# Kernel tuning notes

Hardware: AMD Instinct MI355X
Metric: run time of the kernel (lower is better)

## Reference

```python
import jax, jax.numpy as jnp
import numpy as np

BS, NE, NN, CIN, H, D = 8, 4800, 4981, 3, 128, 6
EPG = 19200
NEDGE = BS * EPG
N = BS * NE

PARAM_NAMES = [
    'enc_cw1','enc_cb1','enc_cw2','enc_cb2','enc_cw3','enc_clng','enc_clnb',
    'enc_ew1','enc_eb1','enc_ew2','enc_eb2','enc_ew3','enc_elng','enc_elnb',
    'p_ew1','p_eb1','p_ew2','p_eb2','p_ew3','p_elng','p_elnb',
    'p_nw1','p_nb1','p_nw2','p_nb2','p_nw3','p_nlng','p_nlnb',
    'dec_uw1','dec_ub1','dec_uw2','dec_ub2','dec_uw3','dec_ulng','dec_ulnb',
    'dec_cw1','dec_cb1','dec_cw2','dec_cb2','dec_cw3']


def setup_inputs():
    key = jax.random.key(0)
    ks = iter(jax.random.split(key, 64))
    def nrm(shape, s=0.1):
        return jax.random.normal(next(ks), shape, jnp.float32) * s
    inp = {}
    inp['x'] = jax.random.normal(next(ks), (BS * NN, CIN), jnp.float32)
    inp['elem_conn'] = jax.random.randint(next(ks), (NE, 4), 0, NN)
    inp['edge_index'] = jax.random.randint(next(ks), (2, NEDGE), 0, N)
    inp['enc_cw1'] = nrm((CIN, 4, 1)); inp['enc_cb1'] = nrm((CIN, 1), 0.01)
    inp['enc_cw2'] = nrm((CIN, 1, 1)); inp['enc_cb2'] = nrm((CIN, 1), 0.01)
    inp['enc_cw3'] = nrm((CIN, 1, 1))
    inp['enc_clng'] = jnp.ones((CIN, 1)); inp['enc_clnb'] = jnp.zeros((CIN, 1))
    inp['enc_ew1'] = nrm((CIN, H)); inp['enc_eb1'] = nrm((H,), 0.01)
    inp['enc_ew2'] = nrm((H, H)); inp['enc_eb2'] = nrm((H,), 0.01)
    inp['enc_ew3'] = nrm((H, H))
    inp['enc_elng'] = jnp.ones((H,)); inp['enc_elnb'] = jnp.zeros((H,))
    inp['p_ew1'] = nrm((D, 2 * H, H)); inp['p_eb1'] = nrm((D, H), 0.01)
    inp['p_ew2'] = nrm((D, H, H)); inp['p_eb2'] = nrm((D, H), 0.01)
    inp['p_ew3'] = nrm((D, H, H))
    inp['p_elng'] = jnp.ones((D, H)); inp['p_elnb'] = jnp.zeros((D, H))
    inp['p_nw1'] = nrm((D, 2 * H, H)); inp['p_nb1'] = nrm((D, H), 0.01)
    inp['p_nw2'] = nrm((D, H, H)); inp['p_nb2'] = nrm((D, H), 0.01)
    inp['p_nw3'] = nrm((D, H, H))
    inp['p_nlng'] = jnp.ones((D, H)); inp['p_nlnb'] = jnp.zeros((D, H))
    inp['dec_uw1'] = nrm((H, 1, 4)); inp['dec_ub1'] = nrm((H, 4), 0.01)
    inp['dec_uw2'] = nrm((H, 4, 4)); inp['dec_ub2'] = nrm((H, 4), 0.01)
    inp['dec_uw3'] = nrm((H, 4, 4))
    inp['dec_ulng'] = jnp.ones((H, 4)); inp['dec_ulnb'] = jnp.zeros((H, 4))
    inp['dec_cw1'] = nrm((H, CIN)); inp['dec_cb1'] = nrm((CIN,), 0.01)
    inp['dec_cw2'] = nrm((CIN, CIN)); inp['dec_cb2'] = nrm((CIN,), 0.01)
    inp['dec_cw3'] = nrm((CIN, CIN))
    return inp


def lrelu(x):
    return jnp.where(x >= 0, x, 0.2 * x)


def ln(x, g, b, axis=-1):
    m = jnp.mean(x, axis=axis, keepdims=True)
    v = jnp.var(x, axis=axis, keepdims=True)
    return (x - m) / jnp.sqrt(v + 1e-5) * g + b


def mlp(x, w1, b1, w2, b2, w3):
    h = lrelu(x @ w1 + b1)
    h = lrelu(h @ w2 + b2)
    return h @ w3


def _forward(fl, elem_conn, edge_index):
    x = fl[0]
    P = dict(zip(PARAM_NAMES, fl[1:]))
    # ---- Encoder: MeshCNN gather (4 mesh nodes per element) + per-channel MLP 4->1 ----
    xg = x.reshape(BS, NN, CIN)[:, elem_conn]                  # (BS, NE, 4, CIN)
    h = lrelu(jnp.einsum('beic,cio->beoc', xg, P['enc_cw1']) + P['enc_cb1'].T[None, None])
    h = lrelu(jnp.einsum('beic,cio->beoc', h, P['enc_cw2']) + P['enc_cb2'].T[None, None])
    h = jnp.einsum('beic,cio->beoc', h, P['enc_cw3'])
    h = ln(h, P['enc_clng'].T[None, None], P['enc_clnb'].T[None, None], axis=2)  # LayerNorm(1)
    h = h[:, :, 0, :].reshape(N, CIN)
    h = ln(mlp(h, P['enc_ew1'], P['enc_eb1'], P['enc_ew2'], P['enc_eb2'], P['enc_ew3']),
           P['enc_elng'], P['enc_elnb'])                       # (N, H)
    # ---- Processor: D GraphNet blocks, edge MLP + scatter-add + node MLP ----
    src, dest = edge_index[0], edge_index[1]
    stacked = (P['p_ew1'], P['p_eb1'], P['p_ew2'], P['p_eb2'], P['p_ew3'], P['p_elng'], P['p_elnb'],
               P['p_nw1'], P['p_nb1'], P['p_nw2'], P['p_nb2'], P['p_nw3'], P['p_nlng'], P['p_nlnb'])
    def step(hc, p):
        ew1, eb1, ew2, eb2, ew3, eg, ebv, nw1, nb1, nw2, nb2, nw3, ng, nbv = p
        msg = jnp.concatenate([hc[dest], hc[src]], axis=-1)    # (NEDGE, 2H)
        m = ln(mlp(msg, ew1, eb1, ew2, eb2, ew3), eg, ebv)
        aggr = jax.ops.segment_sum(m, dest, num_segments=N)
        hn = ln(mlp(jnp.concatenate([hc, aggr], axis=-1), nw1, nb1, nw2, nb2, nw3), ng, nbv)
        return hn, None
    h, _ = jax.lax.scan(step, h, stacked)
    # ---- Decoder: per-channel upsample 1->4 then index_add back to mesh nodes ----
    u = h.reshape(BS, NE, H)[:, :, None, :]                    # (BS, NE, 1, H)
    u = lrelu(jnp.einsum('beic,cio->beoc', u, P['dec_uw1']) + P['dec_ub1'].T[None, None])
    u = lrelu(jnp.einsum('beic,cio->beoc', u, P['dec_uw2']) + P['dec_ub2'].T[None, None])
    u = jnp.einsum('beic,cio->beoc', u, P['dec_uw3'])
    u = ln(u, P['dec_ulng'].T[None, None], P['dec_ulnb'].T[None, None], axis=2)  # (BS, NE, 4, H)
    out = jnp.zeros((BS, NN, H), u.dtype).at[:, elem_conn.reshape(-1)].add(u.reshape(BS, NE * 4, H))
    out = out.reshape(BS * NN, H)
    o = lrelu(out @ P['dec_cw1'] + P['dec_cb1'])
    o = lrelu(o @ P['dec_cw2'] + P['dec_cb2'])
    return o @ P['dec_cw3']


def reference(x, elem_conn, edge_index,
              enc_cw1, enc_cb1, enc_cw2, enc_cb2, enc_cw3, enc_clng, enc_clnb,
              enc_ew1, enc_eb1, enc_ew2, enc_eb2, enc_ew3, enc_elng, enc_elnb,
              p_ew1, p_eb1, p_ew2, p_eb2, p_ew3, p_elng, p_elnb,
              p_nw1, p_nb1, p_nw2, p_nb2, p_nw3, p_nlng, p_nlnb,
              dec_uw1, dec_ub1, dec_uw2, dec_ub2, dec_uw3, dec_ulng, dec_ulnb,
              dec_cw1, dec_cb1, dec_cw2, dec_cb2, dec_cw3):
    fl = (x, enc_cw1, enc_cb1, enc_cw2, enc_cb2, enc_cw3, enc_clng, enc_clnb,
          enc_ew1, enc_eb1, enc_ew2, enc_eb2, enc_ew3, enc_elng, enc_elnb,
          p_ew1, p_eb1, p_ew2, p_eb2, p_ew3, p_elng, p_elnb,
          p_nw1, p_nb1, p_nw2, p_nb2, p_nw3, p_nlng, p_nlnb,
          dec_uw1, dec_ub1, dec_uw2, dec_ub2, dec_uw3, dec_ulng, dec_ulnb,
          dec_cw1, dec_cb1, dec_cw2, dec_cb2, dec_cw3)
    return _forward(fl, elem_conn, edge_index)
```

## Files before the change

### kernel.cpp

```cpp
#include <hip/hip_runtime.h>
#include <hip/hip_fp16.h>
#include <math.h>

#define BS    8
#define NE    4800
#define NN    4981
#define CIN   3
#define HD    128
#define DBLK  6
#define NEDGE 153600
#define NTOT  38400
#define NMESH (BS*NN)
#define NNP   5120
#define EM    128
#define TROWS 256

#define UW1T  0
#define UB1T  512
#define UW2T  1024
#define UB2T  3072
#define UW3T  3584
#define ULNGT 5632
#define ULNBT 6144
#define DWT_N 6656

typedef _Float16 f16;
typedef _Float16 f16x8 __attribute__((ext_vector_type(8)));
typedef float f32x4 __attribute__((ext_vector_type(4)));

__device__ __forceinline__ float lrelu(float x) { return x >= 0.0f ? x : 0.2f * x; }

__global__ __launch_bounds__(128)
void enc_msg0_kernel(const float* __restrict__ clnb,
                     const float* __restrict__ ew1, const float* __restrict__ eb1,
                     const float* __restrict__ ew2, const float* __restrict__ eb2,
                     const float* __restrict__ ew3,
                     const float* __restrict__ g, const float* __restrict__ b,
                     float* __restrict__ hv0,
                     const float* __restrict__ pew1, const float* __restrict__ peb1,
                     const float* __restrict__ pew2, const float* __restrict__ peb2,
                     const float* __restrict__ pew3,
                     const float* __restrict__ pg, const float* __restrict__ pb,
                     float* __restrict__ m0) {
    __shared__ float s1[HD], s2[HD], s3[HD], hv[HD];
    int j = threadIdx.x;
    float a = eb1[j];
    for (int c = 0; c < CIN; ++c) a += clnb[c] * ew1[c * HD + j];
    s1[j] = lrelu(a);
    __syncthreads();
    a = eb2[j];
    for (int k = 0; k < HD; ++k) a += s1[k] * ew2[k * HD + j];
    s2[j] = lrelu(a);
    __syncthreads();
    a = 0.0f;
    for (int k = 0; k < HD; ++k) a += s2[k] * ew3[k * HD + j];
    s3[j] = a;
    __syncthreads();
    float m = 0.0f;
    for (int k = 0; k < HD; ++k) m += s3[k];
    m *= (1.0f / HD);
    float v = 0.0f;
    for (int k = 0; k < HD; ++k) { float d = s3[k] - m; v += d * d; }
    v *= (1.0f / HD);
    float rs = 1.0f / sqrtf(v + 1e-5f);
    float h0 = (s3[j] - m) * rs * g[j] + b[j];
    hv0[j] = h0;
    hv[j] = h0;
    __syncthreads();
    a = peb1[j];
    for (int k = 0; k < HD; ++k) a += hv[k] * (pew1[k * HD + j] + pew1[(k + HD) * HD + j]);
    s1[j] = lrelu(a);
    __syncthreads();
    a = peb2[j];
    for (int k = 0; k < HD; ++k) a += s1[k] * pew2[k * HD + j];
    s2[j] = lrelu(a);
    __syncthreads();
    a = 0.0f;
    for (int k = 0; k < HD; ++k) a += s2[k] * pew3[k * HD + j];
    s3[j] = a;
    __syncthreads();
    m = 0.0f;
    for (int k = 0; k < HD; ++k) m += s3[k];
    m *= (1.0f / HD);
    v = 0.0f;
    for (int k = 0; k < HD; ++k) { float d = s3[k] - m; v += d * d; }
    v *= (1.0f / HD);
    rs = 1.0f / sqrtf(v + 1e-5f);
    m0[j] = (s3[j] - m) * rs * pg[j] + pb[j];
}

__global__ __launch_bounds__(256)
void conv_all_kernel(const float* __restrict__ ew1, const float* __restrict__ ew2,
                     const float* __restrict__ ew3,
                     const float* __restrict__ nw1, const float* __restrict__ nw2,
                     const float* __restrict__ nw3, f16* __restrict__ wbuf,
                     const float* __restrict__ eb1, f16* __restrict__ eb16,
                     const float* __restrict__ uw1, const float* __restrict__ ub1,
                     const float* __restrict__ uw2, const float* __restrict__ ub2,
                     const float* __restrict__ uw3, const float* __restrict__ ulng,
                     const float* __restrict__ ulnb, float* __restrict__ dwt,
                     int* __restrict__ degIota,
                     int* __restrict__ zdeg, int* __restrict__ zcur,
                     int* __restrict__ zmdeg, int* __restrict__ zmcur) {
    int b = blockIdx.x;
    int tid = threadIdx.x;
    if (b == 48) {
        for (int i = tid; i < DBLK * HD; i += 256)
            eb16[i] = (f16)eb1[i];
        degIota[tid] = tid;
        return;
    }
    if (b == 49) {
        for (int idx = tid; idx < 512; idx += 256) {
            int o = idx >> 7, c = idx & 127;
            dwt[UW1T + idx] = uw1[c * 4 + o];
            dwt[UB1T + idx] = ub1[c * 4 + o];
            dwt[UB2T + idx] = ub2[c * 4 + o];
            dwt[ULNGT + idx] = ulng[c * 4 + o];
            dwt[ULNBT + idx] = ulnb[c * 4 + o];
        }
        for (int idx = tid; idx < 2048; idx += 256) {
            int io = idx >> 7, c = idx & 127;
            dwt[UW2T + idx] = uw2[c * 16 + io];
            dwt[UW3T + idx] = uw3[c * 16 + io];
        }
        return;
    }
    if (b >= 50) {
        uint4 z = {0, 0, 0, 0};
        for (int idx = (b - 50) * 256 + tid; idx < 21760; idx += 8 * 256) {
            if (idx < 9600)       ((uint4*)zdeg)[idx] = z;
            else if (idx < 19200) ((uint4*)zcur)[idx - 9600] = z;
            else if (idx < 20480) ((uint4*)zmdeg)[idx - 19200] = z;
            else                  ((uint4*)zmcur)[idx - 20480] = z;
        }
        return;
    }
    int d = b >> 3, m = b & 7;
    const float* src;
    switch (m) {
        case 0: src = ew1 + (size_t)d * 2 * HD * HD; break;
        case 1: src = ew1 + (size_t)d * 2 * HD * HD + HD * HD; break;
        case 2: src = ew2 + (size_t)d * HD * HD; break;
        case 3: src = ew3 + (size_t)d * HD * HD; break;
        case 4: src = nw1 + (size_t)d * 2 * HD * HD; break;
        case 5: src = nw1 + (size_t)d * 2 * HD * HD + HD * HD; break;
        case 6: src = nw2 + (size_t)d * HD * HD; break;
        default: src = nw3 + (size_t)d * HD * HD; break;
    }
    f16* out = wbuf + (size_t)b * HD * HD;
    for (int idx = tid; idx < HD * HD; idx += 256) {
        int n = idx >> 7, k = idx & 127;
        out[idx] = (f16)src[k * HD + n];
    }
}

#define EHB (NEDGE / 256)
#define MHB (NE * 4 / 256)
#define ESB (NTOT / 256)
#define MSB (NNP / 256)

__global__ __launch_bounds__(256)
void prep_hist(const int* __restrict__ e_dst, const int* __restrict__ conn,
               int* __restrict__ deg, int* __restrict__ mdeg) {
    int b = blockIdx.x;
    if (b < EHB) {
        int e = b * 256 + threadIdx.x;
        atomicAdd(&deg[e_dst[e]], 1);
    } else {
        int idx = (b - EHB) * 256 + threadIdx.x;
        atomicAdd(&mdeg[conn[idx]], 1);
    }
}

__device__ __forceinline__ void scan1_body(const int* __restrict__ deg,
                                           int* __restrict__ rowptr,
                                           int* __restrict__ bsum, int bi) {
    __shared__ int s[256];
    int i = bi * 256 + threadIdx.x;
    int v = deg[i];
    s[threadIdx.x] = v;
    __syncthreads();
    for (int off = 1; off < 256; off <<= 1) {
        int t = (threadIdx.x >= off) ? s[threadIdx.x - off] : 0;
        __syncthreads();
        s[threadIdx.x] += t;
        __syncthreads();
    }
    rowptr[i] = s[threadIdx.x] - v;
    if (threadIdx.x == 255) bsum[bi] = s[255];
}

__global__ __launch_bounds__(256)
void prep_scan1(const int* __restrict__ deg, int* __restrict__ rowptr,
                int* __restrict__ bsum,
                const int* __restrict__ mdeg, int* __restrict__ mrow,
                int* __restrict__ mbsum) {
    int b = blockIdx.x;
    if (b < ESB) scan1_body(deg, rowptr, bsum, b);
    else         scan1_body(mdeg, mrow, mbsum, b - ESB);
}

__global__ __launch_bounds__(256)
void prep_scan3(int* __restrict__ rowptr, const int* __restrict__ bsum,
                int* __restrict__ mrow, const int* __restrict__ mbsum) {
    __shared__ int sb[256];
    int b = blockIdx.x;
    int tid = threadIdx.x;
    if (b < ESB) {
        sb[tid] = (tid < b) ? bsum[tid] : 0;
        __syncthreads();
        for (int off = 128; off >= 1; off >>= 1) {
            if (tid < off) sb[tid] += sb[tid + off];
            __syncthreads();
        }
        rowptr[b * 256 + tid] += sb[0];
    } else {
        int bb = b - ESB;
        sb[tid] = (tid < bb) ? mbsum[tid] : 0;
        __syncthreads();
        for (int off = 128; off >= 1; off >>= 1) {
            if (tid < off) sb[tid] += sb[tid + off];
            __syncthreads();
        }
        mrow[bb * 256 + tid] += sb[0];
    }
}

__global__ __launch_bounds__(256)
void prep_scatter(const int* __restrict__ dest, const int* __restrict__ srcv,
                  const int* __restrict__ rowptr, int* __restrict__ cursor,
                  int* __restrict__ dsorted, int* __restrict__ ssorted,
                  const int* __restrict__ conn, const int* __restrict__ mrow,
                  int* __restrict__ mcur, int* __restrict__ mslot,
                  const int* __restrict__ deg,
                  int* __restrict__ ddegs, int* __restrict__ sdegs) {
    int b = blockIdx.x;
    if (b < EHB) {
        int e = b * 256 + threadIdx.x;
        int d = dest[e];
        int s = srcv[e];
        int pos = rowptr[d] + atomicAdd(&cursor[d], 1);
        dsorted[pos] = d;
        ssorted[pos] = s;
        ddegs[pos] = deg[d];
        sdegs[pos] = deg[s];
    } else {
        int idx = (b - EHB) * 256 + threadIdx.x;
        int nd = conn[idx];
        int pos = mrow[nd] + atomicAdd(&mcur[nd], 1);
        mslot[pos] = idx;
    }
}

template <int NT>
__device__ __forceinline__ void stage_w(const f16* __restrict__ Wg, f16 (*Bt)[HD + 8],
                                        int tid) {
    #pragma unroll
    for (int t = 0; t < 2048 / NT; ++t) {
        int idx = tid + t * NT;
        int r = idx >> 4, c = (idx & 15) * 8;
        *(uint4*)(&Bt[r][c]) = *(const uint4*)(Wg + (size_t)r * HD + c);
    }
}

__device__ __forceinline__ void mfma_pass(const f16 (*A)[HD + 8], const f16 (*Bt)[HD + 8],
                                          int rt_base, int ct_base, int ln, int quad,
                                          f32x4 acc[2][4]) {
    #pragma unroll
    for (int ks = 0; ks < 4; ++ks) {
        int kb = ks * 32 + quad * 8;
        f16x8 a0 = *(const f16x8*)(&A[rt_base + ln][kb]);
        f16x8 a1 = *(const f16x8*)(&A[rt_base + 16 + ln][kb]);
        #pragma unroll
        for (int c = 0; c < 4; ++c) {
            f16x8 b = *(const f16x8*)(&Bt[ct_base + c * 16 + ln][kb]);
            acc[0][c] = __builtin_amdgcn_mfma_f32_16x16x32_f16(a0, b, acc[0][c], 0, 0, 0);
            acc[1][c] = __builtin_amdgcn_mfma_f32_16x16x32_f16(a1, b, acc[1][c], 0, 0, 0);
        }
    }
}

__global__ __launch_bounds__(512, 4)
void gn_edge(const f16* __restrict__ P1, const f16* __restrict__ P2,
             const int* __restrict__ dsorted, const int* __restrict__ ssorted,
             const f16* __restrict__ W2, const f16* __restrict__ W3,
             const f16* __restrict__ b1h, const float* __restrict__ b2,
             const float* __restrict__ g, const float* __restrict__ bln,
             f16* __restrict__ msg) {
    __shared__ __align__(16) f16 As[EM][HD + 8];
    __shared__ __align__(16) f16 Bt[HD][HD + 8];
    __shared__ float red[EM][2][2];

    const int tid = threadIdx.x;
    const int base = blockIdx.x * EM;
    const int wave = tid >> 6, lane = tid & 63;
    const int ln = lane & 15, quad = lane >> 4;
    const int rt_base = (wave >> 1) * 32;
    const int ct_base = (wave & 1) * 64;
    const int half = wave & 1;
    const int r0 = tid >> 4;
    const int cg = (tid & 15) * 8;

    const f16 k02s = (f16)0.2f;
    const f16x8 k02 = {k02s, k02s, k02s, k02s, k02s, k02s, k02s, k02s};

    int dI[4], sI[4];
    #pragma unroll
    for (int it = 0; it < 4; ++it) {
        dI[it] = dsorted[base + r0 + it * 32];
        sI[it] = ssorted[base + r0 + it * 32];
    }
    stage_w<512>(W2, Bt, tid);
    const f16x8 bb = *(const f16x8*)(b1h + cg);
    #pragma unroll
    for (int it = 0; it < 4; ++it) {
        f16x8 p1 = *(const f16x8*)(P1 + (size_t)dI[it] * HD + cg);
        f16x8 p2 = *(const f16x8*)(P2 + (size_t)sI[it] * HD + cg);
        f16x8 s = p1 + p2 + bb;
        *(f16x8*)(&As[r0 + it * 32][cg]) = __builtin_elementwise_max(s, s * k02);
    }
    __syncthreads();

    f32x4 acc[2][4];

    #pragma unroll
    for (int c = 0; c < 4; ++c) {
        float bj = b2[ct_base + c * 16 + ln];
        f32x4 bv = {bj, bj, bj, bj};
        acc[0][c] = bv; acc[1][c] = bv;
    }
    mfma_pass(As, Bt, rt_base, ct_base, ln, quad, acc);
    __syncthreads();
    stage_w<512>(W3, Bt, tid);
    #pragma unroll
    for (int i = 0; i < 2; ++i)
        #pragma unroll
        for (int c = 0; c < 4; ++c)
            #pragma unroll
            for (int r = 0; r < 4; ++r)
                As[rt_base + i * 16 + quad * 4 + r][ct_base + c * 16 + ln] =
                    (f16)lrelu(acc[i][c][r]);
    __syncthreads();

    #pragma unroll
    for (int c = 0; c < 4; ++c) { f32x4 z = {0,0,0,0}; acc[0][c] = z; acc[1][c] = z; }
    mfma_pass(As, Bt, rt_base, ct_base, ln, quad, acc);

    #pragma unroll
    for (int i = 0; i < 2; ++i)
        #pragma unroll
        for (int r = 0; r < 4; ++r) {
            float s = acc[i][0][r] + acc[i][1][r] + acc[i][2][r] + acc[i][3][r];
            float q = acc[i][0][r] * acc[i][0][r] + acc[i][1][r] * acc[i][1][r] +
                      acc[i][2][r] * acc[i][2][r] + acc[i][3][r] * acc[i][3][r];
            s += __shfl_xor(s, 1); q += __shfl_xor(q, 1);
            s += __shfl_xor(s, 2); q += __shfl_xor(q, 2);
            s += __shfl_xor(s, 4); q += __shfl_xor(q, 4);
            s += __shfl_xor(s, 8); q += __shfl_xor(q, 8);
            if (ln == 0) {
                int row = rt_base + i * 16 + quad * 4 + r;
                red[row][half][0] = s;
                red[row][half][1] = q;
            }
        }
    __syncthreads();

    float gv[4], bv[4];
    #pragma unroll
    for (int c = 0; c < 4; ++c) {
        int col = ct_base + c * 16 + ln;
        gv[c] = g[col]; bv[c] = bln[col];
    }
    #pragma unroll
    for (int i = 0; i < 2; ++i)
        #pragma unroll
        for (int r = 0; r < 4; ++r) {
            int row = rt_base + i * 16 + quad * 4 + r;
            float s = red[row][0][0] + red[row][1][0];
            float q = red[row][0][1] + red[row][1][1];
            float m = s * (1.0f / HD);
            float var = q * (1.0f / HD) - m * m;
            float rs = 1.0f / sqrtf(var + 1e-5f);
            #pragma unroll
            for (int c = 0; c < 4; ++c) {
                int col = ct_base + c * 16 + ln;
                float v = (acc[i][c][r] - m) * rs * gv[c] + bv[c];
                msg[(size_t)(base + row) * HD + col] = (f16)v;
            }
        }
}

template <int AGGR, bool PROD, bool DECF, bool HTAB>
__global__ __launch_bounds__(256, 3)
void gn_node(f16* __restrict__ h16, const f16* __restrict__ msg,
             const int* __restrict__ rowptr, const int* __restrict__ deg,
             const float* __restrict__ m0, const float* __restrict__ hv0,
             const f16* __restrict__ htab,
             const f16* __restrict__ W1a, const f16* __restrict__ W1b,
             const f16* __restrict__ W2, const f16* __restrict__ W3,
             const float* __restrict__ b1, const float* __restrict__ b2,
             const float* __restrict__ g, const float* __restrict__ bln,
             const f16* __restrict__ nW1a, const f16* __restrict__ nW1b,
             f16* __restrict__ P1, f16* __restrict__ P2,
             const float* __restrict__ dwt, f16* __restrict__ uval) {
    __shared__ __align__(16) f16 As[64][HD + 8];
    __shared__ __align__(16) f16 Bt[HD][HD + 8];
    __shared__ float red[64][2][2];

    const int tid = threadIdx.x;
    const int base = blockIdx.x * 64;
    const int wave = tid >> 6, lane = tid & 63;
    const int ln = lane & 15, quad = lane >> 4;
    const int rt_base = (wave >> 1) * 32;
    const int ct_base = (wave & 1) * 64;
    const int half = wave & 1;

    f16x8 hreg[4];
    #pragma unroll
    for (int t = 0; t < 4; ++t) {
        int r = (tid >> 4) + t * 16;
        int c = (tid & 15) * 8;
        if (AGGR == 0) {
            f16x8 hz;
            #pragma unroll
            for (int u = 0; u < 8; ++u) hz[u] = (f16)hv0[c + u];
            hreg[t] = hz;
            float sc = (float)deg[base + r];
            f16x8 o;
            #pragma unroll
            for (int u = 0; u < 8; ++u) o[u] = (f16)(sc * m0[c + u]);
            *(f16x8*)(&As[r][c]) = o;
        } else {
            if (HTAB)
                hreg[t] = *(const f16x8*)(htab + (size_t)deg[base + r] * HD + c);
            else
                hreg[t] = *(const f16x8*)(h16 + (size_t)(base + r) * HD + c);
            int rp = rowptr[base + r], dg = deg[base + r];
            float a[8] = {0, 0, 0, 0, 0, 0, 0, 0};
            int j = 0;
            for (; j + 4 <= dg; j += 4) {
                f16x8 v0 = *(const f16x8*)(msg + (size_t)(rp + j) * HD + c);
                f16x8 v1 = *(const f16x8*)(msg + (size_t)(rp + j + 1) * HD + c);
                f16x8 v2 = *(const f16x8*)(msg + (size_t)(rp + j + 2) * HD + c);
                f16x8 v3 = *(const f16x8*)(msg + (size_t)(rp + j + 3) * HD + c);
                #pragma unroll
                for (int u = 0; u < 8; ++u)
                    a[u] += ((float)v0[u] + (float)v1[u]) + ((float)v2[u] + (float)v3[u]);
            }
            for (; j < dg; ++j) {
                f16x8 mv = *(const f16x8*)(msg + (size_t)(rp + j) * HD + c);
                #pragma unroll
                for (int u = 0; u < 8; ++u) a[u] += (float)mv[u];
            }
            f16x8 o;
            #pragma unroll
            for (int u = 0; u < 8; ++u) o[u] = (f16)a[u];
            *(f16x8*)(&As[r][c]) = o;
        }
    }
    stage_w<256>(W1b, Bt, tid);
    __syncthreads();

    f32x4 acc[2][4];
    #pragma unroll
    for (int c = 0; c < 4; ++c) {
        float bj = b1[ct_base + c * 16 + ln];
        f32x4 bb = {bj, bj, bj, bj};
        acc[0][c] = bb; acc[1][c] = bb;
    }
    mfma_pass(As, Bt, rt_base, ct_base, ln, quad, acc);
    __syncthreads();

    #pragma unroll
    for (int t = 0; t < 4; ++t) {
        int r = (tid >> 4) + t * 16;
        int c = (tid & 15) * 8;
        *(f16x8*)(&As[r][c]) = hreg[t];
    }
    stage_w<256>(W1a, Bt, tid);
    __syncthreads();
    mfma_pass(As, Bt, rt_base, ct_base, ln, quad, acc);
    __syncthreads();

    stage_w<256>(W2, Bt, tid);
    #pragma unroll
    for (int i = 0; i < 2; ++i)
        #pragma unroll
        for (int c = 0; c < 4; ++c)
            #pragma unroll
            for (int r = 0; r < 4; ++r)
                As[rt_base + i * 16 + quad * 4 + r][ct_base + c * 16 + ln] =
                    (f16)lrelu(acc[i][c][r]);
    __syncthreads();

    #pragma unroll
    for (int c = 0; c < 4; ++c) {
        float bj = b2[ct_base + c * 16 + ln];
        f32x4 bb = {bj, bj, bj, bj};
        acc[0][c] = bb; acc[1][c] = bb;
    }
    mfma_pass(As, Bt, rt_base, ct_base, ln, quad, acc);
    __syncthreads();
    stage_w<256>(W3, Bt, tid);
    #pragma unroll
    for (int i = 0; i < 2; ++i)
        #pragma unroll
        for (int c = 0; c < 4; ++c)
            #pragma unroll
            for (int r = 0; r < 4; ++r)
                As[rt_base + i * 16 + quad * 4 + r][ct_base + c * 16 + ln] =
                    (f16)lrelu(acc[i][c][r]);
    __syncthreads();

    #pragma unroll
    for (int c = 0; c < 4; ++c) { f32x4 z = {0,0,0,0}; acc[0][c] = z; acc[1][c] = z; }
    mfma_pass(As, Bt, rt_base, ct_base, ln, quad, acc);

    #pragma unroll
    for (int i = 0; i < 2; ++i)
        #pragma unroll
        for (int r = 0; r < 4; ++r) {
            float s = acc[i][0][r] + acc[i][1][r] + acc[i][2][r] + acc[i][3][r];
            float q = acc[i][0][r] * acc[i][0][r] + acc[i][1][r] * acc[i][1][r] +
                      acc[i][2][r] * acc[i][2][r] + acc[i][3][r] * acc[i][3][r];
            s += __shfl_xor(s, 1); q += __shfl_xor(q, 1);
            s += __shfl_xor(s, 2); q += __shfl_xor(q, 2);
            s += __shfl_xor(s, 4); q += __shfl_xor(q, 4);
            s += __shfl_xor(s, 8); q += __shfl_xor(q, 8);
            if (ln == 0) {
                int row = rt_base + i * 16 + quad * 4 + r;
                red[row][half][0] = s;
                red[row][half][1] = q;
            }
        }
    __syncthreads();

    float gv[4], bv[4];
    #pragma unroll
    for (int c = 0; c < 4; ++c) {
        int col = ct_base + c * 16 + ln;
        gv[c] = g[col]; bv[c] = bln[col];
    }

    if (!DECF) {
        #pragma unroll
        for (int i = 0; i < 2; ++i)
            #pragma unroll
            for (int r = 0; r < 4; ++r) {
                int row = rt_base + i * 16 + quad * 4 + r;
                float s = red[row][0][0] + red[row][1][0];
                float q = red[row][0][1] + red[row][1][1];
                float m = s * (1.0f / HD);
                float var = q * (1.0f / HD) - m * m;
                float rs = 1.0f / sqrtf(var + 1e-5f);
                #pragma unroll
                for (int c = 0; c < 4; ++c) {
                    int col = ct_base + c * 16 + ln;
                    float v = (acc[i][c][r] - m) * rs * gv[c] + bv[c];
                    f16 hv = (f16)v;
                    h16[(size_t)(base + row) * HD + col] = hv;
                    if (PROD) As[row][col] = hv;
                }
            }
    } else {
        float mm[2][4], rr[2][4];
        #pragma unroll
        for (int i = 0; i < 2; ++i)
            #pragma unroll
            for (int r = 0; r < 4; ++r) {
                int row = rt_base + i * 16 + quad * 4 + r;
                float s = red[row][0][0] + red[row][1][0];
                float q = red[row][0][1] + red[row][1][1];
                float m = s * (1.0f / HD);
                float var = q * (1.0f / HD) - m * m;
                mm[i][r] = m;
                rr[i][r] = 1.0f / sqrtf(var + 1e-5f);
            }
        #pragma unroll
        for (int c = 0; c < 4; ++c) {
            int col = ct_base + c * 16 + ln;
            float w1v[4], wb1[4], wb2[4], lg4[4], lb4[4];
            #pragma unroll
            for (int o = 0; o < 4; ++o) {
                w1v[o] = dwt[UW1T + o * 128 + col];
                wb1[o] = dwt[UB1T + o * 128 + col];
                wb2[o] = dwt[UB2T + o * 128 + col];
                lg4[o] = dwt[ULNGT + o * 128 + col];
                lb4[o] = dwt[ULNBT + o * 128 + col];
            }
            float w2v[16], w3v[16];
            #pragma unroll
            for (int io = 0; io < 16; ++io) {
                w2v[io] = dwt[UW2T + io * 128 + col];
                w3v[io] = dwt[UW3T + io * 128 + col];
            }
            #pragma unroll
            for (int i = 0; i < 2; ++i)
                #pragma unroll
                for (int r = 0; r < 4; ++r) {
                    int row = rt_base + i * 16 + quad * 4 + r;
                    float v = (acc[i][c][r] - mm[i][r]) * rr[i][r] * gv[c] + bv[c];
                    float s = (float)(f16)v;
                    float u1[4], u2[4], u3[4];
                    #pragma unroll
                    for (int o = 0; o < 4; ++o)
                        u1[o] = lrelu(s * w1v[o] + wb1[o]);
                    #pragma unroll
                    for (int o = 0; o < 4; ++o) {
                        float a = wb2[o];
                        #pragma unroll
                        for (int i2 = 0; i2 < 4; ++i2) a += u1[i2] * w2v[i2 * 4 + o];
                        u2[o] = lrelu(a);
                    }
                    #pragma unroll
                    for (int o = 0; o < 4; ++o) {
                        float a = 0.f;
                        #pragma unroll
                        for (int i2 = 0; i2 < 4; ++i2) a += u2[i2] * w3v[i2 * 4 + o];
                        u3[o] = a;
                    }
                    float m4 = 0.25f * (u3[0] + u3[1] + u3[2] + u3[3]);
                    float var4 = 0.f;
                    #pragma unroll
                    for (int o = 0; o < 4; ++o) { float d = u3[o] - m4; var4 += d * d; }
                    var4 *= 0.25f;
                    float rs4 = 1.0f / sqrtf(var4 + 1e-5f);
                    size_t ub = (size_t)(base + row) * 4 * HD + col;
                    #pragma unroll
                    for (int o = 0; o < 4; ++o)
                        uval[ub + (size_t)o * HD] =
                            (f16)((u3[o] - m4) * rs4 * lg4[o] + lb4[o]);
                }
        }
    }

    if (PROD) {
        __syncthreads();
        stage_w<256>(nW1a, Bt, tid);
        __syncthreads();
        #pragma unroll
        for (int c = 0; c < 4; ++c) { f32x4 z = {0,0,0,0}; acc[0][c] = z; acc[1][c] = z; }
        mfma_pass(As, Bt, rt_base, ct_base, ln, quad, acc);
        #pragma unroll
        for (int i = 0; i < 2; ++i)
            #pragma unroll
            for (int c = 0; c < 4; ++c)
                #pragma unroll
                for (int r = 0; r < 4; ++r)
                    P1[(size_t)(base + rt_base + i * 16 + quad * 4 + r) * HD +
                       ct_base + c * 16 + ln] = (f16)acc[i][c][r];
        __syncthreads();
        stage_w<256>(nW1b, Bt, tid);
        __syncthreads();
        #pragma unroll
        for (int c = 0; c < 4; ++c) { f32x4 z = {0,0,0,0}; acc[0][c] = z; acc[1][c] = z; }
        mfma_pass(As, Bt, rt_base, ct_base, ln, quad, acc);
        #pragma unroll
        for (int i = 0; i < 2; ++i)
            #pragma unroll
            for (int c = 0; c < 4; ++c)
                #pragma unroll
                for (int r = 0; r < 4; ++r)
                    P2[(size_t)(base + rt_base + i * 16 + quad * 4 + r) * HD +
                       ct_base + c * 16 + ln] = (f16)acc[i][c][r];
    }
}

__global__ __launch_bounds__(256)
void dec_gather_out(const f16* __restrict__ uval,
                    const int* __restrict__ mrow, const int* __restrict__ mdeg,
                    const int* __restrict__ mslot,
                    const float* __restrict__ cw1, const float* __restrict__ cb1,
                    const float* __restrict__ cw2, const float* __restrict__ cb2,
                    const float* __restrict__ cw3,
                    float* __restrict__ o, int nrows) {
    int r = blockIdx.x * 4 + (threadIdx.x >> 6);
    if (r >= nrows) return;
    int lane = threadIdx.x & 63;
    int b = r / NN, n = r - b * NN;
    int rp = mrow[n], dg = mdeg[n];
    size_t boff = (size_t)b * NE * 4;
    float a0 = 0.f, a1 = 0.f;
    int j = 0;
    for (; j + 4 <= dg; j += 4) {
        int s0 = mslot[rp + j], s1 = mslot[rp + j + 1];
        int s2 = mslot[rp + j + 2], s3 = mslot[rp + j + 3];
        const f16* u0 = uval + (boff + s0) * HD + lane * 2;
        const f16* u1 = uval + (boff + s1) * HD + lane * 2;
        const f16* u2 = uval + (boff + s2) * HD + lane * 2;
        const f16* u3 = uval + (boff + s3) * HD + lane * 2;
        float b00 = (float)u0[0], b01 = (float)u0[1];
        float b10 = (float)u1[0], b11 = (float)u1[1];
        float b20 = (float)u2[0], b21 = (float)u2[1];
        float b30 = (float)u3[0], b31 = (float)u3[1];
        a0 += (b00 + b10) + (b20 + b30);
        a1 += (b01 + b11) + (b21 + b31);
    }
    for (; j < dg; ++j) {
        int slot = mslot[rp + j];
        const f16* up = uval + (boff + slot) * HD + lane * 2;
        a0 += (float)up[0];
        a1 += (float)up[1];
    }
    int c0 = lane * 2, c1 = lane * 2 + 1;
    float s[3];
    #pragma unroll
    for (int k = 0; k < 3; ++k)
        s[k] = a0 * cw1[c0 * 3 + k] + a1 * cw1[c1 * 3 + k];
    #pragma unroll
    for (int off = 32; off >= 1; off >>= 1) {
        s[0] += __shfl_down(s[0], off);
        s[1] += __shfl_down(s[1], off);
        s[2] += __shfl_down(s[2], off);
    }
    if (lane == 0) {
        float t1[3], t2[3];
        #pragma unroll
        for (int k = 0; k < 3; ++k) t1[k] = lrelu(s[k] + cb1[k]);
        #pragma unroll
        for (int k = 0; k < 3; ++k) {
            float a = cb2[k];
            #pragma unroll
            for (int q = 0; q < 3; ++q) a += t1[q] * cw2[q * 3 + k];
            t2[k] = lrelu(a);
        }
        #pragma unroll
        for (int k = 0; k < 3; ++k) {
            float a = 0.f;
            #pragma unroll
            for (int q = 0; q < 3; ++q) a += t2[q] * cw3[q * 3 + k];
            o[(size_t)r * 3 + k] = a;
        }
    }
}

extern "C" void kernel_launch(void* const* d_in, const int* in_sizes, int n_in,
                              void* d_out, int out_size, void* d_ws, size_t ws_size,
                              hipStream_t stream) {
    const int* elem_conn = (const int*)d_in[1];
    const int* edge_index = (const int*)d_in[2];
    const int* e_src = edge_index;
    const int* e_dst = edge_index + NEDGE;
    const float* enc_clnb = (const float*)d_in[9];
    const float* enc_ew1 = (const float*)d_in[10];
    const float* enc_eb1 = (const float*)d_in[11];
    const float* enc_ew2 = (const float*)d_in[12];
    const float* enc_eb2 = (const float*)d_in[13];
    const float* enc_ew3 = (const float*)d_in[14];
    const float* enc_elng = (const float*)d_in[15];
    const float* enc_elnb = (const float*)d_in[16];
    const float* p_ew1 = (const float*)d_in[17];
    const float* p_eb1 = (const float*)d_in[18];
    const float* p_ew2 = (const float*)d_in[19];
    const float* p_eb2 = (const float*)d_in[20];
    const float* p_ew3 = (const float*)d_in[21];
    const float* p_elng = (const float*)d_in[22];
    const float* p_elnb = (const float*)d_in[23];
    const float* p_nw1 = (const float*)d_in[24];
    const float* p_nb1 = (const float*)d_in[25];
    const float* p_nw2 = (const float*)d_in[26];
    const float* p_nb2 = (const float*)d_in[27];
    const float* p_nw3 = (const float*)d_in[28];
    const float* p_nlng = (const float*)d_in[29];
    const float* p_nlnb = (const float*)d_in[30];
    const float* dec_uw1 = (const float*)d_in[31];
    const float* dec_ub1 = (const float*)d_in[32];
    const float* dec_uw2 = (const float*)d_in[33];
    const float* dec_ub2 = (const float*)d_in[34];
    const float* dec_uw3 = (const float*)d_in[35];
    const float* dec_ulng = (const float*)d_in[36];
    const float* dec_ulnb = (const float*)d_in[37];
    const float* dec_cw1 = (const float*)d_in[38];
    const float* dec_cb1 = (const float*)d_in[39];
    const float* dec_cw2 = (const float*)d_in[40];
    const float* dec_cb2 = (const float*)d_in[41];
    const float* dec_cw3 = (const float*)d_in[42];

    char* ws = (char*)d_ws;
    f16*   h16     = (f16*)(ws);
    f16*   wbuf    = (f16*)(ws + 9830400);
    float* hv0     = (float*)(ws + 11403264);
    float* m0      = (float*)(ws + 11403776);
    f16*   P1      = (f16*)(ws + 11404288);
    f16*   P2      = (f16*)(ws + 21234688);
    f16*   msg     = (f16*)(ws + 31065088);
    int*   deg     = (int*)(ws + 70386688);
    int*   rowptr  = (int*)(ws + 70540288);
    int*   cursor  = (int*)(ws + 70693888);
    int*   bsum    = (int*)(ws + 70847488);
    int*   dsorted = (int*)(ws + 70848512);
    int*   ssorted = (int*)(ws + 71462912);
    f16*   eb16    = (f16*)(ws + 72077312);
    int*   mdeg    = (int*)(ws + 72078848);
    int*   mrow    = (int*)(ws + 72099328);
    int*   mcur    = (int*)(ws + 72119808);
    int*   mbsum   = (int*)(ws + 72140288);
    int*   mslot   = (int*)(ws + 72141312);
    float* dwt     = (float*)(ws + 72218112);
    f16*   uval    = (f16*)(ws + 72244736);
    int*   ddegs   = (int*)(ws + 111566336);
    int*   sdegs   = (int*)(ws + 112180736);
    f16*   tabH    = (f16*)(ws + 112795136);
    f16*   tabP1   = (f16*)(ws + 112860672);
    f16*   tabP2   = (f16*)(ws + 112926208);
    int*   degIota = (int*)(ws + 112991744);

    enc_msg0_kernel<<<1, 128, 0, stream>>>(
        enc_clnb, enc_ew1, enc_eb1, enc_ew2, enc_eb2, enc_ew3, enc_elng, enc_elnb, hv0,
        p_ew1, p_eb1, p_ew2, p_eb2, p_ew3, p_elng, p_elnb, m0);
    conv_all_kernel<<<58, 256, 0, stream>>>(p_ew1, p_ew2, p_ew3,
                                            p_nw1, p_nw2, p_nw3, wbuf, p_eb1, eb16,
                                            dec_uw1, dec_ub1, dec_uw2, dec_ub2,
                                            dec_uw3, dec_ulng, dec_ulnb, dwt,
                                            degIota, deg, cursor, mdeg, mcur);

    {
        const f16* wd = wbuf;
        const f16* wn = wbuf + (size_t)8 * HD * HD;
        gn_node<0, true, false, false><<<TROWS / 64, 256, 0, stream>>>(
            tabH, nullptr, nullptr, degIota, m0, hv0, nullptr,
            wd + 4 * HD * HD, wd + 5 * HD * HD, wd + 6 * HD * HD, wd + 7 * HD * HD,
            p_nb1, p_nb2, p_nlng, p_nlnb,
            wn + 0 * HD * HD, wn + 1 * HD * HD, tabP1, tabP2, nullptr, nullptr);
    }

    prep_hist<<<EHB + MHB, 256, 0, stream>>>(e_dst, elem_conn, deg, mdeg);
    prep_scan1<<<ESB + MSB, 256, 0, stream>>>(deg, rowptr, bsum, mdeg, mrow, mbsum);
    prep_scan3<<<ESB + MSB, 256, 0, stream>>>(rowptr, bsum, mrow, mbsum);
    prep_scatter<<<EHB + MHB, 256, 0, stream>>>(e_dst, e_src, rowptr, cursor,
                                                dsorted, ssorted,
                                                elem_conn, mrow, mcur, mslot,
                                                deg, ddegs, sdegs);

    for (int d = 1; d < DBLK; ++d) {
        const f16* wd = wbuf + (size_t)d * 8 * HD * HD;
        if (d == 1)
            gn_edge<<<NEDGE / EM, 512, 0, stream>>>(
                tabP1, tabP2, ddegs, sdegs,
                wd + 2 * HD * HD, wd + 3 * HD * HD,
                eb16 + (size_t)d * HD, p_eb2 + (size_t)d * HD,
                p_elng + (size_t)d * HD, p_elnb + (size_t)d * HD, msg);
        else
            gn_edge<<<NEDGE / EM, 512, 0, stream>>>(
                P1, P2, dsorted, ssorted,
                wd + 2 * HD * HD, wd + 3 * HD * HD,
                eb16 + (size_t)d * HD, p_eb2 + (size_t)d * HD,
                p_elng + (size_t)d * HD, p_elnb + (size_t)d * HD, msg);
        if (d == 1) {
            const f16* wn = wbuf + (size_t)(d + 1) * 8 * HD * HD;
            gn_node<1, true, false, true><<<NTOT / 64, 256, 0, stream>>>(
                h16, msg, rowptr, deg, nullptr, nullptr, tabH,
                wd + 4 * HD * HD, wd + 5 * HD * HD, wd + 6 * HD * HD, wd + 7 * HD * HD,
                p_nb1 + (size_t)d * HD, p_nb2 + (size_t)d * HD,
                p_nlng + (size_t)d * HD, p_nlnb + (size_t)d * HD,
                wn + 0 * HD * HD, wn + 1 * HD * HD, P1, P2, nullptr, nullptr);
        } else if (d < DBLK - 1) {
            const f16* wn = wbuf + (size_t)(d + 1) * 8 * HD * HD;
            gn_node<1, true, false, false><<<NTOT / 64, 256, 0, stream>>>(
                h16, msg, rowptr, deg, nullptr, nullptr, nullptr,
                wd + 4 * HD * HD, wd + 5 * HD * HD, wd + 6 * HD * HD, wd + 7 * HD * HD,
                p_nb1 + (size_t)d * HD, p_nb2 + (size_t)d * HD,
                p_nlng + (size_t)d * HD, p_nlnb + (size_t)d * HD,
                wn + 0 * HD * HD, wn + 1 * HD * HD, P1, P2, nullptr, nullptr);
        } else {
            gn_node<1, false, true, false><<<NTOT / 64, 256, 0, stream>>>(
                h16, msg, rowptr, deg, nullptr, nullptr, nullptr,
                wd + 4 * HD * HD, wd + 5 * HD * HD, wd + 6 * HD * HD, wd + 7 * HD * HD,
                p_nb1 + (size_t)d * HD, p_nb2 + (size_t)d * HD,
                p_nlng + (size_t)d * HD, p_nlnb + (size_t)d * HD,
                wbuf, wbuf, P1, P2, dwt, uval);
        }
    }

    dec_gather_out<<<(NMESH + 3) / 4, 256, 0, stream>>>(
        uval, mrow, mdeg, mslot, dec_cw1, dec_cb1, dec_cw2, dec_cb2, dec_cw3,
        (float*)d_out, NMESH);
}
```

Baseline: 565.8 us.

## Recompute decoder upsample MLP inside gather kernel instead of storing uval

Moves the per-element 1->4->4->4 upsample MLP and its layer norm out of the last gn_node epilogue and into dec_gather_out, which now reads h16 directly and recomputes the upsampled values per incident slot. This removes writing and re-reading the 4x larger uval buffer (about 39 MB of f16). In exchange each gather recomputes the small MLP per incoming slot (about 4 times redundant) and holds many weight registers per thread, which may lower occupancy.

```diff
diff --git a/kernel.cpp b/kernel.cpp
--- a/kernel.cpp
+++ b/kernel.cpp
@@ -26,6 +26,7 @@
 
 typedef _Float16 f16;
 typedef _Float16 f16x8 __attribute__((ext_vector_type(8)));
+typedef _Float16 f16x2 __attribute__((ext_vector_type(2)));
 typedef float f32x4 __attribute__((ext_vector_type(4)));
 
 __device__ __forceinline__ float lrelu(float x) { return x >= 0.0f ? x : 0.2f * x; }
@@ -391,7 +392,7 @@
         }
 }
 
-template <int AGGR, bool PROD, bool DECF, bool HTAB>
+template <int AGGR, bool PROD, bool HTAB>
 __global__ __launch_bounds__(256, 3)
 void gn_node(f16* __restrict__ h16, const f16* __restrict__ msg,
              const int* __restrict__ rowptr, const int* __restrict__ deg,
@@ -402,8 +403,7 @@
              const float* __restrict__ b1, const float* __restrict__ b2,
              const float* __restrict__ g, const float* __restrict__ bln,
              const f16* __restrict__ nW1a, const f16* __restrict__ nW1b,
-             f16* __restrict__ P1, f16* __restrict__ P2,
-             const float* __restrict__ dwt, f16* __restrict__ uval) {
+             f16* __restrict__ P1, f16* __restrict__ P2) {
     __shared__ __align__(16) f16 As[64][HD + 8];
     __shared__ __align__(16) f16 Bt[HD][HD + 8];
     __shared__ float red[64][2][2];
@@ -542,98 +542,25 @@
         int col = ct_base + c * 16 + ln;
         gv[c] = g[col]; bv[c] = bln[col];
     }
-
-    if (!DECF) {
-        #pragma unroll
-        for (int i = 0; i < 2; ++i)
-            #pragma unroll
-            for (int r = 0; r < 4; ++r) {
-                int row = rt_base + i * 16 + quad * 4 + r;
-                float s = red[row][0][0] + red[row][1][0];
-                float q = red[row][0][1] + red[row][1][1];
-                float m = s * (1.0f / HD);
-                float var = q * (1.0f / HD) - m * m;
-                float rs = 1.0f / sqrtf(var + 1e-5f);
-                #pragma unroll
-                for (int c = 0; c < 4; ++c) {
-                    int col = ct_base + c * 16 + ln;
-                    float v = (acc[i][c][r] - m) * rs * gv[c] + bv[c];
-                    f16 hv = (f16)v;
-                    h16[(size_t)(base + row) * HD + col] = hv;
-                    if (PROD) As[row][col] = hv;
-                }
+    #pragma unroll
+    for (int i = 0; i < 2; ++i)
+        #pragma unroll
+        for (int r = 0; r < 4; ++r) {
+            int row = rt_base + i * 16 + quad * 4 + r;
+            float s = red[row][0][0] + red[row][1][0];
+            float q = red[row][0][1] + red[row][1][1];
+            float m = s * (1.0f / HD);
+            float var = q * (1.0f / HD) - m * m;
+            float rs = 1.0f / sqrtf(var + 1e-5f);
+            #pragma unroll
+            for (int c = 0; c < 4; ++c) {
+                int col = ct_base + c * 16 + ln;
+                float v = (acc[i][c][r] - m) * rs * gv[c] + bv[c];
+                f16 hv = (f16)v;
+                h16[(size_t)(base + row) * HD + col] = hv;
+                if (PROD) As[row][col] = hv;
             }
-    } else {
-        float mm[2][4], rr[2][4];
-        #pragma unroll
-        for (int i = 0; i < 2; ++i)
-            #pragma unroll
-            for (int r = 0; r < 4; ++r) {
-                int row = rt_base + i * 16 + quad * 4 + r;
-                float s = red[row][0][0] + red[row][1][0];
-                float q = red[row][0][1] + red[row][1][1];
-                float m = s * (1.0f / HD);
-                float var = q * (1.0f / HD) - m * m;
-                mm[i][r] = m;
-                rr[i][r] = 1.0f / sqrtf(var + 1e-5f);
-            }
-        #pragma unroll
-        for (int c = 0; c < 4; ++c) {
-            int col = ct_base + c * 16 + ln;
-            float w1v[4], wb1[4], wb2[4], lg4[4], lb4[4];
-            #pragma unroll
-            for (int o = 0; o < 4; ++o) {
-                w1v[o] = dwt[UW1T + o * 128 + col];
-                wb1[o] = dwt[UB1T + o * 128 + col];
-                wb2[o] = dwt[UB2T + o * 128 + col];
-                lg4[o] = dwt[ULNGT + o * 128 + col];
-                lb4[o] = dwt[ULNBT + o * 128 + col];
-            }
-            float w2v[16], w3v[16];
-            #pragma unroll
-            for (int io = 0; io < 16; ++io) {
-                w2v[io] = dwt[UW2T + io * 128 + col];
-                w3v[io] = dwt[UW3T + io * 128 + col];
-            }
-            #pragma unroll
-            for (int i = 0; i < 2; ++i)
-                #pragma unroll
-                for (int r = 0; r < 4; ++r) {
-                    int row = rt_base + i * 16 + quad * 4 + r;
-                    float v = (acc[i][c][r] - mm[i][r]) * rr[i][r] * gv[c] + bv[c];
-                    float s = (float)(f16)v;
-                    float u1[4], u2[4], u3[4];
-                    #pragma unroll
-                    for (int o = 0; o < 4; ++o)
-                        u1[o] = lrelu(s * w1v[o] + wb1[o]);
-                    #pragma unroll
-                    for (int o = 0; o < 4; ++o) {
-                        float a = wb2[o];
-                        #pragma unroll
-                        for (int i2 = 0; i2 < 4; ++i2) a += u1[i2] * w2v[i2 * 4 + o];
-                        u2[o] = lrelu(a);
-                    }
-                    #pragma unroll
-                    for (int o = 0; o < 4; ++o) {
-                        float a = 0.f;
-                        #pragma unroll
-                        for (int i2 = 0; i2 < 4; ++i2) a += u2[i2] * w3v[i2 * 4 + o];
-                        u3[o] = a;
-                    }
-                    float m4 = 0.25f * (u3[0] + u3[1] + u3[2] + u3[3]);
-                    float var4 = 0.f;
-                    #pragma unroll
-                    for (int o = 0; o < 4; ++o) { float d = u3[o] - m4; var4 += d * d; }
-                    var4 *= 0.25f;
-                    float rs4 = 1.0f / sqrtf(var4 + 1e-5f);
-                    size_t ub = (size_t)(base + row) * 4 * HD + col;
-                    #pragma unroll
-                    for (int o = 0; o < 4; ++o)
-                        uval[ub + (size_t)o * HD] =
-                            (f16)((u3[o] - m4) * rs4 * lg4[o] + lb4[o]);
-                }
-        }
-    }
+        }
 
     if (PROD) {
         __syncthreads();
@@ -667,8 +594,39 @@
     }
 }
 
+#define UPSAMPLE(SVAL, W1, B1, B2W, W2V, W3V, LG, LB, OO, OUT)                  \
+    {                                                                           \
+        float u1_[4], u2_[4], u3_[4];                                           \
+        _Pragma("unroll")                                                       \
+        for (int o_ = 0; o_ < 4; ++o_) u1_[o_] = lrelu((SVAL) * W1[o_] + B1[o_]); \
+        _Pragma("unroll")                                                       \
+        for (int o_ = 0; o_ < 4; ++o_) {                                        \
+            float a_ = B2W[o_];                                                 \
+            _Pragma("unroll")                                                   \
+            for (int i_ = 0; i_ < 4; ++i_) a_ += u1_[i_] * W2V[i_ * 4 + o_];    \
+            u2_[o_] = lrelu(a_);                                                \
+        }                                                                       \
+        _Pragma("unroll")                                                       \
+        for (int o_ = 0; o_ < 4; ++o_) {                                        \
+            float a_ = 0.f;                                                     \
+            _Pragma("unroll")                                                   \
+            for (int i_ = 0; i_ < 4; ++i_) a_ += u2_[i_] * W3V[i_ * 4 + o_];    \
+            u3_[o_] = a_;                                                       \
+        }                                                                       \
+        float m4_ = 0.25f * (u3_[0] + u3_[1] + u3_[2] + u3_[3]);                \
+        float v4_ = 0.f;                                                        \
+        _Pragma("unroll")                                                       \
+        for (int o_ = 0; o_ < 4; ++o_) { float d_ = u3_[o_] - m4_; v4_ += d_ * d_; } \
+        v4_ *= 0.25f;                                                           \
+        float rs4_ = 1.0f / sqrtf(v4_ + 1e-5f);                                 \
+        float u3o_ = (OO) == 0 ? u3_[0] : (OO) == 1 ? u3_[1] : (OO) == 2 ? u3_[2] : u3_[3]; \
+        float lgo_ = (OO) == 0 ? LG[0] : (OO) == 1 ? LG[1] : (OO) == 2 ? LG[2] : LG[3]; \
+        float lbo_ = (OO) == 0 ? LB[0] : (OO) == 1 ? LB[1] : (OO) == 2 ? LB[2] : LB[3]; \
+        OUT = (float)(f16)((u3o_ - m4_) * rs4_ * lgo_ + lbo_);                  \
+    }
+
 __global__ __launch_bounds__(256)
-void dec_gather_out(const f16* __restrict__ uval,
+void dec_gather_out(const f16* __restrict__ h16, const float* __restrict__ dwt,
                     const int* __restrict__ mrow, const int* __restrict__ mdeg,
                     const int* __restrict__ mslot,
                     const float* __restrict__ cw1, const float* __restrict__ cb1,
@@ -680,30 +638,56 @@
     int lane = threadIdx.x & 63;
     int b = r / NN, n = r - b * NN;
     int rp = mrow[n], dg = mdeg[n];
-    size_t boff = (size_t)b * NE * 4;
+    size_t ebase = (size_t)b * NE;
+    int c0 = lane * 2, c1 = c0 + 1;
+
+    float w1a[4], w1b[4], b1a[4], b1b[4], b2a[4], b2b[4];
+    float lga[4], lgb[4], lba[4], lbb[4];
+    float w2a[16], w2b[16], w3a[16], w3b[16];
+    #pragma unroll
+    for (int t = 0; t < 4; ++t) {
+        w1a[t] = dwt[UW1T + t * 128 + c0];  w1b[t] = dwt[UW1T + t * 128 + c1];
+        b1a[t] = dwt[UB1T + t * 128 + c0];  b1b[t] = dwt[UB1T + t * 128 + c1];
+        b2a[t] = dwt[UB2T + t * 128 + c0];  b2b[t] = dwt[UB2T + t * 128 + c1];
+        lga[t] = dwt[ULNGT + t * 128 + c0]; lgb[t] = dwt[ULNGT + t * 128 + c1];
+        lba[t] = dwt[ULNBT + t * 128 + c0]; lbb[t] = dwt[ULNBT + t * 128 + c1];
+    }
+    #pragma unroll
+    for (int t = 0; t < 16; ++t) {
+        w2a[t] = dwt[UW2T + t * 128 + c0];  w2b[t] = dwt[UW2T + t * 128 + c1];
+        w3a[t] = dwt[UW3T + t * 128 + c0];  w3b[t] = dwt[UW3T + t * 128 + c1];
+    }
+
     float a0 = 0.f, a1 = 0.f;
     int j = 0;
     for (; j + 4 <= dg; j += 4) {
-        int s0 = mslot[rp + j], s1 = mslot[rp + j + 1];
+        int s0 = mslot[rp + j],     s1 = mslot[rp + j + 1];
         int s2 = mslot[rp + j + 2], s3 = mslot[rp + j + 3];
-        const f16* u0 = uval + (boff + s0) * HD + lane * 2;
-        const f16* u1 = uval + (boff + s1) * HD + lane * 2;
-        const f16* u2 = uval + (boff + s2) * HD + lane * 2;
-        const f16* u3 = uval + (boff + s3) * HD + lane * 2;
-        float b00 = (float)u0[0], b01 = (float)u0[1];
-        float b10 = (float)u1[0], b11 = (float)u1[1];
-        float b20 = (float)u2[0], b21 = (float)u2[1];
-        float b30 = (float)u3[0], b31 = (float)u3[1];
-        a0 += (b00 + b10) + (b20 + b30);
-        a1 += (b01 + b11) + (b21 + b31);
+        f16x2 p0 = *(const f16x2*)(h16 + (ebase + (s0 >> 2)) * HD + c0);
+        f16x2 p1 = *(const f16x2*)(h16 + (ebase + (s1 >> 2)) * HD + c0);
+        f16x2 p2 = *(const f16x2*)(h16 + (ebase + (s2 >> 2)) * HD + c0);
+        f16x2 p3 = *(const f16x2*)(h16 + (ebase + (s3 >> 2)) * HD + c0);
+        float v0a, v0b, v1a, v1b, v2a, v2b, v3a, v3b;
+        UPSAMPLE((float)p0[0], w1a, b1a, b2a, w2a, w3a, lga, lba, (s0 & 3), v0a);
+        UPSAMPLE((float)p0[1], w1b, b1b, b2b, w2b, w3b, lgb, lbb, (s0 & 3), v0b);
+        UPSAMPLE((float)p1[0], w1a, b1a, b2a, w2a, w3a, lga, lba, (s1 & 3), v1a);
+        UPSAMPLE((float)p1[1], w1b, b1b, b2b, w2b, w3b, lgb, lbb, (s1 & 3), v1b);
+        UPSAMPLE((float)p2[0], w1a, b1a, b2a, w2a, w3a, lga, lba, (s2 & 3), v2a);
+        UPSAMPLE((float)p2[1], w1b, b1b, b2b, w2b, w3b, lgb, lbb, (s2 & 3), v2b);
+        UPSAMPLE((float)p3[0], w1a, b1a, b2a, w2a, w3a, lga, lba, (s3 & 3), v3a);
+        UPSAMPLE((float)p3[1], w1b, b1b, b2b, w2b, w3b, lgb, lbb, (s3 & 3), v3b);
+        a0 += (v0a + v1a) + (v2a + v3a);
+        a1 += (v0b + v1b) + (v2b + v3b);
     }
     for (; j < dg; ++j) {
         int slot = mslot[rp + j];
-        const f16* up = uval + (boff + slot) * HD + lane * 2;
-        a0 += (float)up[0];
-        a1 += (float)up[1];
-    }
-    int c0 = lane * 2, c1 = lane * 2 + 1;
+        f16x2 p = *(const f16x2*)(h16 + (ebase + (slot >> 2)) * HD + c0);
+        float va, vb;
+        UPSAMPLE((float)p[0], w1a, b1a, b2a, w2a, w3a, lga, lba, (slot & 3), va);
+        UPSAMPLE((float)p[1], w1b, b1b, b2b, w2b, w3b, lgb, lbb, (slot & 3), vb);
+        a0 += va;
+        a1 += vb;
+    }
     float s[3];
     #pragma unroll
     for (int k = 0; k < 3; ++k)
@@ -798,13 +782,12 @@
     int*   mbsum   = (int*)(ws + 72140288);
     int*   mslot   = (int*)(ws + 72141312);
     float* dwt     = (float*)(ws + 72218112);
-    f16*   uval    = (f16*)(ws + 72244736);
-    int*   ddegs   = (int*)(ws + 111566336);
-    int*   sdegs   = (int*)(ws + 112180736);
-    f16*   tabH    = (f16*)(ws + 112795136);
-    f16*   tabP1   = (f16*)(ws + 112860672);
-    f16*   tabP2   = (f16*)(ws + 112926208);
-    int*   degIota = (int*)(ws + 112991744);
+    int*   ddegs   = (int*)(ws + 72244736);
+    int*   sdegs   = (int*)(ws + 72859136);
+    f16*   tabH    = (f16*)(ws + 73473536);
+    f16*   tabP1   = (f16*)(ws + 73539072);
+    f16*   tabP2   = (f16*)(ws + 73604608);
+    int*   degIota = (int*)(ws + 73670144);
 
     enc_msg0_kernel<<<1, 128, 0, stream>>>(
         enc_clnb, enc_ew1, enc_eb1, enc_ew2, enc_eb2, enc_ew3, enc_elng, enc_elnb, hv0,
@@ -818,11 +801,11 @@
     {
         const f16* wd = wbuf;
         const f16* wn = wbuf + (size_t)8 * HD * HD;
-        gn_node<0, true, false, false><<<TROWS / 64, 256, 0, stream>>>(
+        gn_node<0, true, false><<<TROWS / 64, 256, 0, stream>>>(
             tabH, nullptr, nullptr, degIota, m0, hv0, nullptr,
             wd + 4 * HD * HD, wd + 5 * HD * HD, wd + 6 * HD * HD, wd + 7 * HD * HD,
             p_nb1, p_nb2, p_nlng, p_nlnb,
-            wn + 0 * HD * HD, wn + 1 * HD * HD, tabP1, tabP2, nullptr, nullptr);
+            wn + 0 * HD * HD, wn + 1 * HD * HD, tabP1, tabP2);
     }
 
     prep_hist<<<EHB + MHB, 256, 0, stream>>>(e_dst, elem_conn, deg, mdeg);
@@ -849,31 +832,31 @@
                 p_elng + (size_t)d * HD, p_elnb + (size_t)d * HD, msg);
         if (d == 1) {
             const f16* wn = wbuf + (size_t)(d + 1) * 8 * HD * HD;
-            gn_node<1, true, false, true><<<NTOT / 64, 256, 0, stream>>>(
+            gn_node<1, true, true><<<NTOT / 64, 256, 0, stream>>>(
                 h16, msg, rowptr, deg, nullptr, nullptr, tabH,
                 wd + 4 * HD * HD, wd + 5 * HD * HD, wd + 6 * HD * HD, wd + 7 * HD * HD,
                 p_nb1 + (size_t)d * HD, p_nb2 + (size_t)d * HD,
                 p_nlng + (size_t)d * HD, p_nlnb + (size_t)d * HD,
-                wn + 0 * HD * HD, wn + 1 * HD * HD, P1, P2, nullptr, nullptr);
+                wn + 0 * HD * HD, wn + 1 * HD * HD, P1, P2);
         } else if (d < DBLK - 1) {
             const f16* wn = wbuf + (size_t)(d + 1) * 8 * HD * HD;
-            gn_node<1, true, false, false><<<NTOT / 64, 256, 0, stream>>>(
+            gn_node<1, true, false><<<NTOT / 64, 256, 0, stream>>>(
                 h16, msg, rowptr, deg, nullptr, nullptr, nullptr,
                 wd + 4 * HD * HD, wd + 5 * HD * HD, wd + 6 * HD * HD, wd + 7 * HD * HD,
                 p_nb1 + (size_t)d * HD, p_nb2 + (size_t)d * HD,
                 p_nlng + (size_t)d * HD, p_nlnb + (size_t)d * HD,
-                wn + 0 * HD * HD, wn + 1 * HD * HD, P1, P2, nullptr, nullptr);
+                wn + 0 * HD * HD, wn + 1 * HD * HD, P1, P2);
         } else {
-            gn_node<1, false, true, false><<<NTOT / 64, 256, 0, stream>>>(
+            gn_node<1, false, false><<<NTOT / 64, 256, 0, stream>>>(
                 h16, msg, rowptr, deg, nullptr, nullptr, nullptr,
                 wd + 4 * HD * HD, wd + 5 * HD * HD, wd + 6 * HD * HD, wd + 7 * HD * HD,
                 p_nb1 + (size_t)d * HD, p_nb2 + (size_t)d * HD,
                 p_nlng + (size_t)d * HD, p_nlnb + (size_t)d * HD,
-                wbuf, wbuf, P1, P2, dwt, uval);
+                wbuf, wbuf, P1, P2);
         }
     }
 
     dec_gather_out<<<(NMESH + 3) / 4, 256, 0, stream>>>(
-        uval, mrow, mdeg, mslot, dec_cw1, dec_cb1, dec_cw2, dec_cb2, dec_cw3,
+        h16, dwt, mrow, mdeg, mslot, dec_cw1, dec_cb1, dec_cw2, dec_cb2, dec_cw3,
         (float*)d_out, NMESH);
 }
```

Result: slower. 778.2 us (+37.5%).
